# Kernel tuning notes

Measured on AMD Instinct MI355X. Metric: run time of the kernel, lower is better.

The kernel has to match this reference:

```python
import jax, jax.numpy as jnp
import numpy as np

B, N, D_MODEL, H, BLK = 2, 2048, 1024, 16, 128
TB = N // BLK  # 16 blocks per side
NEG = -1e30


def setup_inputs() -> dict:
    key = jax.random.key(0)
    kq, kk, kv, kb = jax.random.split(key, 4)
    q = jax.random.normal(kq, (B, N, D_MODEL), jnp.float32)
    k = jax.random.normal(kk, (B, N, D_MODEL), jnp.float32)
    v = jax.random.normal(kv, (B, N, D_MODEL), jnp.float32)
    tau = jnp.float32(1.0)
    mask = jnp.ones((B, 1, N, N), jnp.int32)
    block_sparse_mask = jax.random.randint(kb, (TB, TB), 0, 2).astype(jnp.int32)
    return {"q": q, "k": k, "v": v, "tau": tau, "mask": mask,
            "block_sparse_mask": block_sparse_mask}


def reference(q, k, v, tau, mask, block_sparse_mask):
    # Equivalent closed form of the tiled online-softmax loop (dropout p=0, eval
    # mode): processed blocks accumulate exactly masked softmax(tau*QK^T/sqrt(dk))@V;
    # rows whose every block is skipped keep O=0, l=0, m=-inf.
    Bq, Nq, D = q.shape
    d_k = D // H
    qh = q.reshape(Bq, Nq, H, d_k).transpose(0, 2, 1, 3)  # (B,H,N,dk)
    kh = k.reshape(Bq, Nq, H, d_k).transpose(0, 2, 1, 3)
    vh = v.reshape(Bq, Nq, H, d_k).transpose(0, 2, 1, 3)

    S = tau * jnp.einsum('bhqd,bhkd->bhqk', qh, kh) / np.sqrt(d_k).astype(np.float32)

    # expand block-sparse pattern to token resolution (N,N)
    bs = jnp.repeat(jnp.repeat(block_sparse_mask, BLK, axis=0), BLK, axis=1)
    allowed = (mask != 0) & (bs != 0)  # (B,1,N,N), broadcasts over heads

    S_m = jnp.where(allowed, S, NEG)
    m = jnp.max(S_m, axis=-1, keepdims=True)            # (B,H,N,1)
    P = jnp.exp(S_m - m) * allowed.astype(S.dtype)      # masked exp-weights
    l = jnp.sum(P, axis=-1, keepdims=True)              # (B,H,N,1)
    Ov = jnp.einsum('bhqk,bhkd->bhqd', P, vh)
    O = Ov / jnp.where(l > 0, l, 1.0)

    has_any = jnp.any(allowed, axis=-1, keepdims=True)  # (B,1,N,1)
    m_out = jnp.where(has_any, m, -jnp.inf)
    O_out = O.transpose(0, 2, 1, 3).reshape(Bq, Nq, D)
    return O_out, l, m_out
```

## Files before the change

kernel.cpp:

```cpp
#include <hip/hip_runtime.h>
#include <hip/hip_bf16.h>

#define B_   2
#define N_   2048
#define DM_  1024
#define H_   16
#define DK_  64
#define BLK_ 128
#define TB_  16

typedef unsigned short u16;
typedef unsigned int   u32;
using bf16x8 = __attribute__((ext_vector_type(8))) __bf16;
using f32x4  = __attribute__((ext_vector_type(4))) float;

#define KPAD 72
#define VPAD 136
#define PPAD 136
#define OPAD 68

__device__ __forceinline__ u32 pack_bf16(float a, float b) {
  __hip_bfloat162 h = __float22bfloat162_rn(make_float2(a, b));
  u32 u; __builtin_memcpy(&u, &h, 4); return u;
}
__device__ __forceinline__ bf16x8 pack8(float4 f0, float4 f1, float sc) {
  u32 w[4];
  w[0] = pack_bf16(f0.x * sc, f0.y * sc); w[1] = pack_bf16(f0.z * sc, f0.w * sc);
  w[2] = pack_bf16(f1.x * sc, f1.y * sc); w[3] = pack_bf16(f1.z * sc, f1.w * sc);
  bf16x8 r; __builtin_memcpy(&r, w, 16); return r;
}

__global__ void kv_convert(const float* __restrict__ k, const float* __restrict__ v,
                           u16* __restrict__ kb, u16* __restrict__ vt) {
  __shared__ u16 tile[BLK_][DK_ + 2];
  const int b = blockIdx.z, h = blockIdx.y, nb = blockIdx.x;
  const int t = threadIdx.x;
  const int rr = t >> 4, cc = (t & 15) * 4;
  {
    const float* kg = k + ((size_t)(b * N_ + nb * BLK_)) * DM_ + h * DK_;
    u16* kd = kb + ((size_t)((b * H_ + h) * N_) + nb * BLK_) * DK_;
#pragma unroll
    for (int i = 0; i < 8; ++i) {
      const int r = rr + i * 16;
      const float4 f = *(const float4*)(kg + (size_t)r * DM_ + cc);
      *(uint2*)(kd + r * DK_ + cc) = make_uint2(pack_bf16(f.x, f.y), pack_bf16(f.z, f.w));
    }
  }
  {
    const float* vg = v + ((size_t)(b * N_ + nb * BLK_)) * DM_ + h * DK_;
#pragma unroll
    for (int i = 0; i < 8; ++i) {
      const int r = rr + i * 16;
      const float4 f = *(const float4*)(vg + (size_t)r * DM_ + cc);
      *(u32*)(&tile[r][cc])     = pack_bf16(f.x, f.y);
      *(u32*)(&tile[r][cc + 2]) = pack_bf16(f.z, f.w);
    }
    __syncthreads();
    const int d = t >> 2, n0 = (t & 3) * 32;
    u16* og = vt + ((size_t)(b * H_ + h) * DK_ + d) * N_ + nb * BLK_ + n0;
#pragma unroll
    for (int j = 0; j < 32; j += 8) {
      u16 tmp[8];
#pragma unroll
      for (int x = 0; x < 8; ++x) tmp[x] = tile[n0 + j + x][d];
      uint4 w; __builtin_memcpy(&w, tmp, 16);
      *(uint4*)(og + j) = w;
    }
  }
}

__global__ void mask_flags_kernel(const int* __restrict__ mask, const int* __restrict__ bs,
                                  int* __restrict__ flags) {
  const int blk = blockIdx.x;
  const int kb = blk % TB_, qb = (blk / TB_) % TB_, b = blk / (TB_ * TB_);
  const int t = threadIdx.x;
  const int* mg = mask + (size_t)b * N_ * N_ + (size_t)(qb * BLK_) * N_ + kb * BLK_;
  int all1 = 1, any1 = 0;
  for (int i = t; i < BLK_ * BLK_ / 4; i += 256) {
    const int r = i >> 5, c = (i & 31) * 4;
    const int4 mv = *(const int4*)(mg + (size_t)r * N_ + c);
    all1 &= (mv.x != 0) & (mv.y != 0) & (mv.z != 0) & (mv.w != 0);
    any1 |= (mv.x != 0) | (mv.y != 0) | (mv.z != 0) | (mv.w != 0);
  }
  __shared__ int sAll[4], sAny[4];
  const int wv = t >> 6;
  const int wAll = __all(all1), wAny = __any(any1);
  if ((t & 63) == 0) { sAll[wv] = wAll; sAny[wv] = wAny; }
  __syncthreads();
  if (t == 0) {
    const int A = sAll[0] & sAll[1] & sAll[2] & sAll[3];
    const int O = sAny[0] | sAny[1] | sAny[2] | sAny[3];
    int f = 0;
    if (bs[qb * TB_ + kb] != 0 && O) f = A ? 1 : 2;
    flags[blk] = f;
  }
}

__global__ __launch_bounds__(256, 2)
void attn_kernel(const float* __restrict__ q_, const u16* __restrict__ kb_,
                 const u16* __restrict__ vt, const float* __restrict__ tau_p,
                 const int* __restrict__ mask, const int* __restrict__ flags,
                 float* __restrict__ o_out, float* __restrict__ l_out,
                 float* __restrict__ m_out) {
  __shared__ __align__(16) u16 lds[BLK_ * KPAD + DK_ * VPAD + BLK_ * PPAD];
  u16* Ks  = lds;
  u16* Vts = Ks + BLK_ * KPAD;
  u16* Ps  = Vts + DK_ * VPAD;
  float* Os = (float*)lds;

  const int idx = blockIdx.x;
  const int bh = idx & 31, qb128 = idx >> 5;
  const int b = bh >> 4, h = bh & 15;
  const int t = threadIdx.x;
  const int wave = t >> 6, lane = t & 63, quad = lane >> 4, col = lane & 15;

  const int* flg = flags + (b * TB_ + qb128) * TB_;
  u32 actmask = 0, mixmask = 0;
#pragma unroll
  for (int i = 0; i < TB_; ++i) {
    const int f = flg[i];
    actmask |= (f != 0) ? (1u << i) : 0u;
    mixmask |= (f == 2) ? (1u << i) : 0u;
  }

  int qg[2];
  qg[0] = qb128 * BLK_ + wave * 32 + col;
  qg[1] = qg[0] + 16;

  const float qscale = tau_p[0] * 0.125f * 1.44269504f;
  bf16x8 bq[2][2];
#pragma unroll
  for (int nt = 0; nt < 2; ++nt) {
    const float* qr = q_ + ((size_t)(b * N_ + qg[nt])) * DM_ + h * DK_;
#pragma unroll
    for (int half = 0; half < 2; ++half) {
      const float4 f0 = *(const float4*)(qr + half * 32 + quad * 8);
      const float4 f1 = *(const float4*)(qr + half * 32 + quad * 8 + 4);
      bq[nt][half] = pack8(f0, f1, qscale);
    }
  }

  float m_run[2] = {-INFINITY, -INFINITY};
  float l_run[2] = {0.f, 0.f};
  f32x4 oacc[2][4];
#pragma unroll
  for (int nt = 0; nt < 2; ++nt)
#pragma unroll
    for (int mt = 0; mt < 4; ++mt) oacc[nt][mt] = (f32x4){0.f, 0.f, 0.f, 0.f};

  const u16* kbase = kb_ + (size_t)(b * H_ + h) * N_ * DK_;
  const u16* vbase = vt + (size_t)(b * H_ + h) * DK_ * N_;

  u32 rem = actmask;
  while (rem) {
    const int cur = (int)__builtin_ctz(rem);
    rem &= rem - 1;
    const int mix = (mixmask >> cur) & 1;

    __syncthreads();
    {
      const u16* ks = kbase + (size_t)cur * BLK_ * DK_;
      const u16* vs = vbase + cur * BLK_;
      uint4 kr[4], vr[4];
#pragma unroll
      for (int j = 0; j < 4; ++j) {
        const int i = t + 256 * j;
        kr[j] = *(const uint4*)(ks + i * 8);
        vr[j] = *(const uint4*)(vs + (size_t)(i >> 4) * N_ + (i & 15) * 8);
      }
#pragma unroll
      for (int j = 0; j < 4; ++j) {
        const int i = t + 256 * j;
        *(uint4*)(Ks + (i >> 3) * KPAD + (i & 7) * 8) = kr[j];
        *(uint4*)(Vts + (i >> 4) * VPAD + (i & 15) * 8) = vr[j];
      }
    }
    __syncthreads();

#pragma unroll
    for (int nt = 0; nt < 2; ++nt) {
      f32x4 st[8];
#pragma unroll
      for (int kt = 0; kt < 8; ++kt) {
        const bf16x8 a0 = *(const bf16x8*)(Ks + (kt * 16 + col) * KPAD + quad * 8);
        const bf16x8 a1 = *(const bf16x8*)(Ks + (kt * 16 + col) * KPAD + 32 + quad * 8);
        f32x4 c = (f32x4){0.f, 0.f, 0.f, 0.f};
        c = __builtin_amdgcn_mfma_f32_16x16x32_bf16(a0, bq[nt][0], c, 0, 0, 0);
        c = __builtin_amdgcn_mfma_f32_16x16x32_bf16(a1, bq[nt][1], c, 0, 0, 0);
        st[kt] = c;
      }
      if (mix) {
        const int* mg = mask + (size_t)b * N_ * N_ + (size_t)qg[nt] * N_ + cur * BLK_;
#pragma unroll
        for (int kt = 0; kt < 8; ++kt) {
          const int4 mv = *(const int4*)(mg + kt * 16 + quad * 4);
          if (!mv.x) st[kt][0] = -1e30f;
          if (!mv.y) st[kt][1] = -1e30f;
          if (!mv.z) st[kt][2] = -1e30f;
          if (!mv.w) st[kt][3] = -1e30f;
        }
      }
      float mx = -INFINITY;
#pragma unroll
      for (int kt = 0; kt < 8; ++kt)
        mx = fmaxf(mx, fmaxf(fmaxf(st[kt][0], st[kt][1]), fmaxf(st[kt][2], st[kt][3])));
      mx = fmaxf(mx, __shfl_xor(mx, 16, 64));
      mx = fmaxf(mx, __shfl_xor(mx, 32, 64));
      const float mnew = fmaxf(m_run[nt], mx);
      const float alpha = __builtin_amdgcn_exp2f(m_run[nt] - mnew);
      const int qloc = wave * 32 + nt * 16 + col;
      float s = 0.f;
      if (!mix) {
#pragma unroll
        for (int kt = 0; kt < 8; ++kt) {
          const float p0 = __builtin_amdgcn_exp2f(st[kt][0] - mnew);
          const float p1 = __builtin_amdgcn_exp2f(st[kt][1] - mnew);
          const float p2 = __builtin_amdgcn_exp2f(st[kt][2] - mnew);
          const float p3 = __builtin_amdgcn_exp2f(st[kt][3] - mnew);
          s += (p0 + p1) + (p2 + p3);
          *(uint2*)(Ps + qloc * PPAD + kt * 16 + quad * 4) =
              make_uint2(pack_bf16(p0, p1), pack_bf16(p2, p3));
        }
      } else {
#pragma unroll
        for (int kt = 0; kt < 8; ++kt) {
          const float p0 = st[kt][0] <= -1e29f ? 0.f : __builtin_amdgcn_exp2f(st[kt][0] - mnew);
          const float p1 = st[kt][1] <= -1e29f ? 0.f : __builtin_amdgcn_exp2f(st[kt][1] - mnew);
          const float p2 = st[kt][2] <= -1e29f ? 0.f : __builtin_amdgcn_exp2f(st[kt][2] - mnew);
          const float p3 = st[kt][3] <= -1e29f ? 0.f : __builtin_amdgcn_exp2f(st[kt][3] - mnew);
          s += (p0 + p1) + (p2 + p3);
          *(uint2*)(Ps + qloc * PPAD + kt * 16 + quad * 4) =
              make_uint2(pack_bf16(p0, p1), pack_bf16(p2, p3));
        }
      }
      s += __shfl_xor(s, 16, 64);
      s += __shfl_xor(s, 32, 64);
      l_run[nt] = alpha * l_run[nt] + s;
      m_run[nt] = mnew;
#pragma unroll
      for (int mt = 0; mt < 4; ++mt)
#pragma unroll
        for (int r = 0; r < 4; ++r) oacc[nt][mt][r] *= alpha;
    }

#pragma unroll
    for (int ks = 0; ks < 4; ++ks) {
      bf16x8 bfrag[2];
#pragma unroll
      for (int nt = 0; nt < 2; ++nt)
        bfrag[nt] = *(const bf16x8*)(Ps + (wave * 32 + nt * 16 + col) * PPAD + ks * 32 + quad * 8);
#pragma unroll
      for (int mt = 0; mt < 4; ++mt) {
        const bf16x8 av = *(const bf16x8*)(Vts + (mt * 16 + col) * VPAD + ks * 32 + quad * 8);
#pragma unroll
        for (int nt = 0; nt < 2; ++nt)
          oacc[nt][mt] = __builtin_amdgcn_mfma_f32_16x16x32_bf16(av, bfrag[nt], oacc[nt][mt], 0, 0, 0);
      }
    }
  }

  __syncthreads();
#pragma unroll
  for (int nt = 0; nt < 2; ++nt) {
    const float inv = l_run[nt] > 0.f ? 1.f / l_run[nt] : 1.f;
    const int qloc = wave * 32 + nt * 16 + col;
#pragma unroll
    for (int mt = 0; mt < 4; ++mt) {
      float4 w = make_float4(oacc[nt][mt][0] * inv, oacc[nt][mt][1] * inv,
                             oacc[nt][mt][2] * inv, oacc[nt][mt][3] * inv);
      *(float4*)(Os + qloc * OPAD + mt * 16 + quad * 4) = w;
    }
  }
  __syncthreads();
  float* ob = o_out + ((size_t)(b * N_ + qb128 * BLK_)) * DM_ + h * DK_;
#pragma unroll
  for (int j = 0; j < 8; ++j) {
    const int i = t + 256 * j;
    const int r = i >> 4, c4 = (i & 15) * 4;
    const float4 w = *(const float4*)(Os + r * OPAD + c4);
    *(float4*)(ob + (size_t)r * DM_ + c4) = w;
  }
  if (quad == 0) {
#pragma unroll
    for (int nt = 0; nt < 2; ++nt) {
      const size_t oi = (size_t)(b * H_ + h) * N_ + qg[nt];
      l_out[oi] = l_run[nt];
      m_out[oi] = l_run[nt] > 0.f ? m_run[nt] * 0.69314718056f : -INFINITY;
    }
  }
}

extern "C" void kernel_launch(void* const* d_in, const int* in_sizes, int n_in,
                              void* d_out, int out_size, void* d_ws, size_t ws_size,
                              hipStream_t stream) {
  const float* q   = (const float*)d_in[0];
  const float* k   = (const float*)d_in[1];
  const float* v   = (const float*)d_in[2];
  const float* tau = (const float*)d_in[3];
  const int* mask  = (const int*)d_in[4];
  const int* bs    = (const int*)d_in[5];
  float* out = (float*)d_out;

  const size_t plane = (size_t)B_ * H_ * N_ * DK_;
  u16* kb = (u16*)d_ws;
  u16* vt = kb + plane;
  int* flags = (int*)(vt + plane);

  kv_convert<<<dim3(N_ / BLK_, H_, B_), 256, 0, stream>>>(k, v, kb, vt);
  mask_flags_kernel<<<B_ * TB_ * TB_, 256, 0, stream>>>(mask, bs, flags);

  float* o_out = out;
  float* l_out = out + (size_t)B_ * N_ * DM_;
  float* m_out = l_out + (size_t)B_ * H_ * N_;
  attn_kernel<<<dim3(TB_ * 32), 256, 0, stream>>>(q, kb, vt, tau, mask, flags,
                                                  o_out, l_out, m_out);
}
```

Before: 168.2 us.

## Prefetch next K/V block into registers, use lazy softmax rescale and MFMA priority

The attention loop now issues global loads for the next active K/V block into registers before computing the current block, so load latency overlaps with the MFMA and softmax work. The online softmax only rescales the accumulators when some row's max grows by more than 8 (log2 units), and it tracks the true max separately so the final l and m can be corrected. s_setprio raises wave priority around the MFMA sections. The V transpose thread mapping is also changed so that consecutive threads take different d rows. Keeping prefetch registers live raises register pressure, and the skipped rescales let values grow by up to 2^8 before normalization.

```diff
diff --git a/kernel.cpp b/kernel.cpp
--- a/kernel.cpp
+++ b/kernel.cpp
@@ -56,7 +56,7 @@
       *(u32*)(&tile[r][cc + 2]) = pack_bf16(f.z, f.w);
     }
     __syncthreads();
-    const int d = t >> 2, n0 = (t & 3) * 32;
+    const int d = t & 63, n0 = (t >> 6) * 32;
     u16* og = vt + ((size_t)(b * H_ + h) * DK_ + d) * N_ + nb * BLK_ + n0;
 #pragma unroll
     for (int j = 0; j < 32; j += 8) {
@@ -96,6 +96,17 @@
   }
 }
 
+#define ISSUE_KV(blk_) do {                                                     \
+    const u16* ks_ = kbase + (size_t)(blk_) * BLK_ * DK_;                       \
+    const u16* vs_ = vbase + (blk_) * BLK_;                                     \
+    _Pragma("unroll")                                                           \
+    for (int j_ = 0; j_ < 4; ++j_) {                                            \
+      const int i_ = t + 256 * j_;                                              \
+      kr[j_] = *(const uint4*)(ks_ + i_ * 8);                                   \
+      vr[j_] = *(const uint4*)(vs_ + (size_t)(i_ >> 4) * N_ + (i_ & 15) * 8);   \
+    }                                                                           \
+  } while (0)
+
 __global__ __launch_bounds__(256, 2)
 void attn_kernel(const float* __restrict__ q_, const u16* __restrict__ kb_,
                  const u16* __restrict__ vt, const float* __restrict__ tau_p,
@@ -123,6 +134,14 @@
     mixmask |= (f == 2) ? (1u << i) : 0u;
   }
 
+  const u16* kbase = kb_ + (size_t)(b * H_ + h) * N_ * DK_;
+  const u16* vbase = vt + (size_t)(b * H_ + h) * DK_ * N_;
+
+  uint4 kr[4], vr[4];
+  u32 rem = actmask;
+  int cur = -1;
+  if (rem) { cur = (int)__builtin_ctz(rem); rem &= rem - 1; ISSUE_KV(cur); }
+
   int qg[2];
   qg[0] = qb128 * BLK_ + wave * 32 + col;
   qg[1] = qg[0] + 16;
@@ -140,7 +159,8 @@
     }
   }
 
-  float m_run[2] = {-INFINITY, -INFINITY};
+  float m_run[2]  = {-INFINITY, -INFINITY};
+  float m_true[2] = {-INFINITY, -INFINITY};
   float l_run[2] = {0.f, 0.f};
   f32x4 oacc[2][4];
 #pragma unroll
@@ -148,38 +168,25 @@
 #pragma unroll
     for (int mt = 0; mt < 4; ++mt) oacc[nt][mt] = (f32x4){0.f, 0.f, 0.f, 0.f};
 
-  const u16* kbase = kb_ + (size_t)(b * H_ + h) * N_ * DK_;
-  const u16* vbase = vt + (size_t)(b * H_ + h) * DK_ * N_;
-
-  u32 rem = actmask;
-  while (rem) {
-    const int cur = (int)__builtin_ctz(rem);
-    rem &= rem - 1;
+  while (cur >= 0) {
     const int mix = (mixmask >> cur) & 1;
 
     __syncthreads();
-    {
-      const u16* ks = kbase + (size_t)cur * BLK_ * DK_;
-      const u16* vs = vbase + cur * BLK_;
-      uint4 kr[4], vr[4];
-#pragma unroll
-      for (int j = 0; j < 4; ++j) {
-        const int i = t + 256 * j;
-        kr[j] = *(const uint4*)(ks + i * 8);
-        vr[j] = *(const uint4*)(vs + (size_t)(i >> 4) * N_ + (i & 15) * 8);
-      }
-#pragma unroll
-      for (int j = 0; j < 4; ++j) {
-        const int i = t + 256 * j;
-        *(uint4*)(Ks + (i >> 3) * KPAD + (i & 7) * 8) = kr[j];
-        *(uint4*)(Vts + (i >> 4) * VPAD + (i & 15) * 8) = vr[j];
-      }
+#pragma unroll
+    for (int j = 0; j < 4; ++j) {
+      const int i = t + 256 * j;
+      *(uint4*)(Ks + (i >> 3) * KPAD + (i & 7) * 8) = kr[j];
+      *(uint4*)(Vts + (i >> 4) * VPAD + (i & 15) * 8) = vr[j];
     }
     __syncthreads();
+
+    int nxt = -1;
+    if (rem) { nxt = (int)__builtin_ctz(rem); rem &= rem - 1; ISSUE_KV(nxt); }
 
 #pragma unroll
     for (int nt = 0; nt < 2; ++nt) {
       f32x4 st[8];
+      __builtin_amdgcn_s_setprio(1);
 #pragma unroll
       for (int kt = 0; kt < 8; ++kt) {
         const bf16x8 a0 = *(const bf16x8*)(Ks + (kt * 16 + col) * KPAD + quad * 8);
@@ -189,6 +196,7 @@
         c = __builtin_amdgcn_mfma_f32_16x16x32_bf16(a1, bq[nt][1], c, 0, 0, 0);
         st[kt] = c;
       }
+      __builtin_amdgcn_s_setprio(0);
       if (mix) {
         const int* mg = mask + (size_t)b * N_ * N_ + (size_t)qg[nt] * N_ + cur * BLK_;
 #pragma unroll
@@ -206,8 +214,21 @@
         mx = fmaxf(mx, fmaxf(fmaxf(st[kt][0], st[kt][1]), fmaxf(st[kt][2], st[kt][3])));
       mx = fmaxf(mx, __shfl_xor(mx, 16, 64));
       mx = fmaxf(mx, __shfl_xor(mx, 32, 64));
-      const float mnew = fmaxf(m_run[nt], mx);
-      const float alpha = __builtin_amdgcn_exp2f(m_run[nt] - mnew);
+      m_true[nt] = fmaxf(m_true[nt], mx);
+
+      const float mold = m_run[nt];
+      float mnew = mold;
+      if (!__all(mx <= mold + 8.f)) {
+        mnew = fmaxf(mold, mx);
+        const float alpha = __builtin_amdgcn_exp2f(mold - mnew);
+        l_run[nt] *= alpha;
+#pragma unroll
+        for (int mt = 0; mt < 4; ++mt)
+#pragma unroll
+          for (int r = 0; r < 4; ++r) oacc[nt][mt][r] *= alpha;
+        m_run[nt] = mnew;
+      }
+
       const int qloc = wave * 32 + nt * 16 + col;
       float s = 0.f;
       if (!mix) {
@@ -235,14 +256,10 @@
       }
       s += __shfl_xor(s, 16, 64);
       s += __shfl_xor(s, 32, 64);
-      l_run[nt] = alpha * l_run[nt] + s;
-      m_run[nt] = mnew;
-#pragma unroll
-      for (int mt = 0; mt < 4; ++mt)
-#pragma unroll
-        for (int r = 0; r < 4; ++r) oacc[nt][mt][r] *= alpha;
-    }
-
+      l_run[nt] += s;
+    }
+
+    __builtin_amdgcn_s_setprio(1);
 #pragma unroll
     for (int ks = 0; ks < 4; ++ks) {
       bf16x8 bfrag[2];
@@ -257,6 +274,8 @@
           oacc[nt][mt] = __builtin_amdgcn_mfma_f32_16x16x32_bf16(av, bfrag[nt], oacc[nt][mt], 0, 0, 0);
       }
     }
+    __builtin_amdgcn_s_setprio(0);
+    cur = nxt;
   }
 
   __syncthreads();
@@ -284,8 +303,10 @@
 #pragma unroll
     for (int nt = 0; nt < 2; ++nt) {
       const size_t oi = (size_t)(b * H_ + h) * N_ + qg[nt];
-      l_out[oi] = l_run[nt];
-      m_out[oi] = l_run[nt] > 0.f ? m_run[nt] * 0.69314718056f : -INFINITY;
+      const float lv = l_run[nt] > 0.f
+          ? l_run[nt] * __builtin_amdgcn_exp2f(m_run[nt] - m_true[nt]) : 0.f;
+      l_out[oi] = lv;
+      m_out[oi] = l_run[nt] > 0.f ? m_true[nt] * 0.69314718056f : -INFINITY;
     }
   }
 }
```

New measurement: 193.4 us. 1.15x slower.
